# Kernel optimization log

Hardware: AMD Instinct MI355X
Metric: run time of the kernel (lower is better)

## Reference

```python
import jax, jax.numpy as jnp
import numpy as np

B, C, H, W = 16, 64, 256, 256
WS = 4  # window_size


def setup_inputs() -> dict:
    key = jax.random.key(0)
    k = jax.random.split(key, 5)
    c2, c4 = C // 2, C // 4
    return {
        "x": jax.random.normal(k[0], (B, C, H, W), dtype=jnp.float32),
        "w1": jax.random.normal(k[1], (c2, C), dtype=jnp.float32) * 0.05,
        "b1": jax.random.normal(k[2], (c2,), dtype=jnp.float32) * 0.05,
        "w2": jax.random.normal(k[3], (C, c4), dtype=jnp.float32) * 0.05,
        "b2": jax.random.normal(k[4], (C,), dtype=jnp.float32) * 0.05,
    }


def reference(x, w1, b1, w2, b2):
    b, c, h, w = x.shape
    ws = WS
    c2, c4 = c // 2, c // 4
    bnum = ws * ws                      # 16 windows positions
    l = (h // ws) * (w // ws)           # tokens per position

    # inp: 1x1 conv c->c/2 + ReLU
    x_ = jax.nn.relu(jnp.einsum('oc,bchw->bohw', w1, x) + b1[None, :, None, None])

    # rearrange 'b c (h dh) (w dw) -> b c (dh dw) (h w)', dh=dw=4
    qx = x_.reshape(b, c2, h // ws, ws, w // ws, ws)
    qx = qx.transpose(0, 1, 3, 5, 2, 4).reshape(b, c2, bnum, l)

    vx = qx[:, c4:]                     # [b, c/4, 16, l]

    # windowed mean + (buggy, faithful) 3rd moment: divisor is bnum (dim-2 size), not l
    mean = qx.mean(-1, keepdims=True)                    # [b, c/2, 16, 1]
    m3 = ((qx - mean) ** 3).sum(-1, keepdims=True) / bnum
    qkv = mean + m3

    q, v = qkv[:, :c4], qkv[:, c4:]     # each [b, c/4, 16, 1]

    atn = jax.nn.softmax(q @ jnp.swapaxes(q, -1, -2), axis=-1)  # [b, c/4, 16, 16]
    y = atn @ v                                                 # [b, c/4, 16, 1]

    Fv = vx * jax.nn.sigmoid(y)         # broadcast gate over l

    # inverse rearrange 'b c (dh dw) (h w) -> b c (h dh) (w dw)'
    Fv = Fv.reshape(b, c4, ws, ws, h // ws, w // ws)
    Fv = Fv.transpose(0, 1, 4, 2, 5, 3).reshape(b, c4, h, w)

    out = jnp.einsum('oc,bchw->bohw', w2, Fv) + b2[None, :, None, None]
    return out + x
```

## Files before the change

kernel.cpp:

```cpp
#include <hip/hip_runtime.h>

#define NB 16
#define NC 64
#define C2 32
#define C4 16
#define HH 256
#define WW 256
#define HW (HH*WW)
#define NPIX (NB*NC*HW)


__global__ __launch_bounds__(256) void prep_kernel(const float* __restrict__ w1,
                                                   float* __restrict__ ws) {
    int t = threadIdx.x;
    for (int i = t; i < 24576; i += 256) ws[2048 + i] = 0.f;
    for (int i = t; i < 2048; i += 256) {
        int o = i >> 6, c = i & 63;
        ws[c * 32 + o] = w1[i];
    }
}

__global__ __launch_bounds__(256) void stats_kernel(const float* __restrict__ x,
                                                    const float* __restrict__ w1t,
                                                    const float* __restrict__ b1,
                                                    float* __restrict__ stats) {
    int b     = blockIdx.x >> 6;
    int sub   = blockIdx.x & 63;
    int r     = sub & 3;
    int chunk = sub >> 2;
    int w     = threadIdx.x;
    const float* xb = x + (size_t)b * NC * HW;

    float S1[32], S2[32], S3[32];
    #pragma unroll
    for (int o = 0; o < 32; o++) { S1[o] = 0.f; S2[o] = 0.f; S3[o] = 0.f; }

    for (int i = 0; i < 4; ++i) {
        int h = r + 4 * (chunk * 4 + i);
        const float* xp = xb + h * WW + w;
        float acc[32];
        #pragma unroll
        for (int o = 0; o < 32; o++) acc[o] = b1[o];
        #pragma unroll 8
        for (int c = 0; c < 64; c++) {
            float xc = xp[(size_t)c * HW];
            #pragma unroll
            for (int o = 0; o < 32; o++) acc[o] += w1t[c * 32 + o] * xc;
        }
        #pragma unroll
        for (int o = 0; o < 32; o++) {
            float v = acc[o] > 0.f ? acc[o] : 0.f;
            S1[o] += v;
            float p = v * v;
            S2[o] += p;
            S3[o] += p * v;
        }
    }

    int lane = threadIdx.x & 63;
    #pragma unroll
    for (int o = 0; o < 32; o++) {
        float a = S1[o], bb = S2[o], cc = S3[o];
        #pragma unroll
        for (int m = 4; m <= 32; m <<= 1) {
            a  += __shfl_xor(a,  m);
            bb += __shfl_xor(bb, m);
            cc += __shfl_xor(cc, m);
        }
        if (lane < 4) {
            int si = r * 4 + lane;
            int idx = b * 512 + o * 16 + si;
            atomicAdd(&stats[idx],         a);
            atomicAdd(&stats[8192 + idx],  bb);
            atomicAdd(&stats[16384 + idx], cc);
        }
    }
}

__global__ __launch_bounds__(512) void attn_kernel(const float* __restrict__ stats,
                                                   float* __restrict__ gates) {
    int b = blockIdx.x;
    int t = threadIdx.x;
    __shared__ float qkv[512];
    {
        int idx = b * 512 + t;
        float S1 = stats[idx];
        float S2 = stats[8192 + idx];
        float S3 = stats[16384 + idx];
        float mu = S1 * (1.f / 4096.f);
        float m3 = (S3 - 3.f * mu * S2 + 2.f * 4096.f * mu * mu * mu) * (1.f / 16.f);
        qkv[t] = mu + m3;
    }
    __syncthreads();
    if (t < 256) {
        int o = t >> 4, s = t & 15;
        float qs = qkv[o * 16 + s];
        float mx = -1e30f;
        #pragma unroll
        for (int k = 0; k < 16; k++) mx = fmaxf(mx, qs * qkv[o * 16 + k]);
        float sum = 0.f, y = 0.f;
        #pragma unroll
        for (int k = 0; k < 16; k++) {
            float e = __expf(qs * qkv[o * 16 + k] - mx);
            sum += e;
            y   += e * qkv[(16 + o) * 16 + k];
        }
        y /= sum;
        float g = 1.f / (1.f + __expf(-y));
        gates[b * 256 + o * 16 + s] = g;
    }
}

__global__ __launch_bounds__(256) void out_kernel(const float* __restrict__ x,
                                                  const float* __restrict__ w1t,
                                                  const float* __restrict__ b1,
                                                  const float* __restrict__ w2,
                                                  const float* __restrict__ b2,
                                                  const float* __restrict__ gates,
                                                  float* __restrict__ out) {
    int bh = blockIdx.x;
    int b  = bh >> 8;
    int h  = bh & 255;
    int w  = threadIdx.x;
    int s  = (h & 3) * 4 + (w & 3);
    const float* xb = x   + (size_t)b * NC * HW + h * WW + w;
    float*       ob = out + (size_t)b * NC * HW + h * WW + w;

    __shared__ float gsh[256];
    gsh[w] = gates[b * 256 + w];
    __syncthreads();

    float xr[64];
    #pragma unroll
    for (int c = 0; c < 64; c++) xr[c] = xb[(size_t)c * HW];

    float fv[16];
    #pragma unroll
    for (int j = 0; j < 16; j++) fv[j] = b1[16 + j];
    #pragma unroll
    for (int c = 0; c < 64; c++) {
        float xc = xr[c];
        #pragma unroll
        for (int j = 0; j < 16; j++) fv[j] += w1t[c * 32 + 16 + j] * xc;
    }
    #pragma unroll
    for (int j = 0; j < 16; j++) {
        float v = fv[j] > 0.f ? fv[j] : 0.f;
        fv[j] = v * gsh[j * 16 + s];
    }
    #pragma unroll
    for (int o = 0; o < 64; o++) {
        float r = b2[o] + xr[o];
        #pragma unroll
        for (int j = 0; j < 16; j++) r += w2[o * 16 + j] * fv[j];
        ob[(size_t)o * HW] = r;
    }
}

extern "C" void kernel_launch(void* const* d_in, const int* in_sizes, int n_in,
                              void* d_out, int out_size, void* d_ws, size_t ws_size,
                              hipStream_t stream) {
    const float* x  = (const float*)d_in[0];
    const float* w1 = (const float*)d_in[1];
    const float* b1 = (const float*)d_in[2];
    const float* w2 = (const float*)d_in[3];
    const float* b2 = (const float*)d_in[4];
    float* ws    = (float*)d_ws;
    float* w1t   = ws;
    float* stats = ws + 2048;
    float* gates = ws + 26624;
    float* out   = (float*)d_out;

    prep_kernel <<<1,    256, 0, stream>>>(w1, ws);
    stats_kernel<<<1024, 256, 0, stream>>>(x, w1t, b1, stats);
    attn_kernel <<<16,   512, 0, stream>>>(stats, gates);
    out_kernel  <<<4096, 256, 0, stream>>>(x, w1t, b1, w2, b2, gates, out);
}
```

Before: 269.8 us.

## Double-buffer stats kernel input via async global-to-LDS loads

The stats kernel now stages each row's input channels into shared memory with direct global-to-LDS loads. It uses two buffers, each holding 32 channels, and prefetches the next half-row while the current one is computed. The goal is to overlap memory latency with the 1x1 conv FMAs instead of issuing strided global loads inline. This adds 64KB of LDS per block and barriers each stage, which may lower occupancy.

```diff
diff --git a/kernel.cpp b/kernel.cpp
--- a/kernel.cpp
+++ b/kernel.cpp
@@ -7,7 +7,6 @@
 #define HH 256
 #define WW 256
 #define HW (HH*WW)
-#define NPIX (NB*NC*HW)
 
 
 __global__ __launch_bounds__(256) void prep_kernel(const float* __restrict__ w1,
@@ -20,44 +19,80 @@
     }
 }
 
+__device__ __forceinline__ void gl_lds16(const float* g, float* l) {
+    __builtin_amdgcn_global_load_lds(
+        (const __attribute__((address_space(1))) unsigned int*)g,
+        (__attribute__((address_space(3))) unsigned int*)l,
+        16, 0, 0);
+}
+
 __global__ __launch_bounds__(256) void stats_kernel(const float* __restrict__ x,
                                                     const float* __restrict__ w1t,
                                                     const float* __restrict__ b1,
                                                     float* __restrict__ stats) {
+    __shared__ float lds[2][32 * 256];
+
     int b     = blockIdx.x >> 6;
     int sub   = blockIdx.x & 63;
     int r     = sub & 3;
     int chunk = sub >> 2;
-    int w     = threadIdx.x;
+    int t     = threadIdx.x;
+    int wid   = t >> 6;
+    int lane  = t & 63;
     const float* xb = x + (size_t)b * NC * HW;
 
-    float S1[32], S2[32], S3[32];
+#define STAGE(s_) do {                                                        \
+        int i_ = (s_) >> 1;                                                   \
+        int h_ = r + 4 * (chunk * 4 + i_);                                    \
+        const float* gs_ = xb + (size_t)((s_) & 1) * 32 * HW + (size_t)h_ * WW; \
+        float* ls_ = &lds[(s_) & 1][0];                                       \
+        _Pragma("unroll")                                                     \
+        for (int j_ = 0; j_ < 8; ++j_) {                                      \
+            int cl_ = j_ * 4 + wid;                                           \
+            gl_lds16(gs_ + (size_t)cl_ * HW + lane * 4, ls_ + cl_ * 256);     \
+        }                                                                     \
+    } while (0)
+
+    float acc[32], S1[32], S2[32], S3[32];
     #pragma unroll
     for (int o = 0; o < 32; o++) { S1[o] = 0.f; S2[o] = 0.f; S3[o] = 0.f; }
 
-    for (int i = 0; i < 4; ++i) {
-        int h = r + 4 * (chunk * 4 + i);
-        const float* xp = xb + h * WW + w;
-        float acc[32];
-        #pragma unroll
-        for (int o = 0; o < 32; o++) acc[o] = b1[o];
+    STAGE(0);
+    for (int s = 0; s < 8; ++s) {
+        if (s < 7) {
+            STAGE(s + 1);
+            asm volatile("s_waitcnt vmcnt(8)" ::: "memory");
+        } else {
+            asm volatile("s_waitcnt vmcnt(0)" ::: "memory");
+        }
+        __builtin_amdgcn_s_barrier();
+
+        const float* L = &lds[s & 1][0];
+        int cbase = (s & 1) * 32;
+        if (cbase == 0) {
+            #pragma unroll
+            for (int o = 0; o < 32; o++) acc[o] = b1[o];
+        }
         #pragma unroll 8
-        for (int c = 0; c < 64; c++) {
-            float xc = xp[(size_t)c * HW];
+        for (int c = 0; c < 32; ++c) {
+            float xc = L[c * 256 + t];
             #pragma unroll
-            for (int o = 0; o < 32; o++) acc[o] += w1t[c * 32 + o] * xc;
-        }
-        #pragma unroll
-        for (int o = 0; o < 32; o++) {
-            float v = acc[o] > 0.f ? acc[o] : 0.f;
-            S1[o] += v;
-            float p = v * v;
-            S2[o] += p;
-            S3[o] += p * v;
-        }
-    }
-
-    int lane = threadIdx.x & 63;
+            for (int o = 0; o < 32; o++) acc[o] += w1t[(cbase + c) * 32 + o] * xc;
+        }
+        if (cbase) {
+            #pragma unroll
+            for (int o = 0; o < 32; o++) {
+                float v = acc[o] > 0.f ? acc[o] : 0.f;
+                S1[o] += v;
+                float p = v * v;
+                S2[o] += p;
+                S3[o] += p * v;
+            }
+        }
+        __builtin_amdgcn_s_barrier();
+    }
+#undef STAGE
+
     #pragma unroll
     for (int o = 0; o < 32; o++) {
         float a = S1[o], bb = S2[o], cc = S3[o];
```

Result: no change. 274.7 us (+1.8%).
